# Optimization experiments

Hardware: AMD Instinct MI355X
Metric: run time of the kernel (lower is better)

The kernel has to match this reference:

```python
import jax, jax.numpy as jnp
import numpy as np

B, N, C, H, KS = 4, 1024, 768, 12, 7
DFF = 4 * C
HD = C // H
EPS = 1e-5


def layernorm(x, g, b):
    mu = jnp.mean(x, axis=-1, keepdims=True)
    var = jnp.mean(jnp.square(x - mu), axis=-1, keepdims=True)
    return (x - mu) * jax.lax.rsqrt(var + EPS) * g + b


def setup_inputs() -> dict:
    key = jax.random.key(0)
    ks = jax.random.split(key, 16)
    s = 0.02
    return {
        "x": jax.random.normal(ks[0], (B, N, C), jnp.float32),
        "w_qkv": jax.random.normal(ks[1], (3 * C, C), jnp.float32) * s,
        "b_qkv": jnp.zeros((3 * C,), jnp.float32),
        "w_proj": jax.random.normal(ks[2], (C, C), jnp.float32) * s,
        "b_proj": jnp.zeros((C,), jnp.float32),
        "w_fc1": jax.random.normal(ks[3], (DFF, C), jnp.float32) * s,
        "b_fc1": jnp.zeros((DFF,), jnp.float32),
        "w_fc2": jax.random.normal(ks[4], (C, DFF), jnp.float32) * s,
        "b_fc2": jnp.zeros((C,), jnp.float32),
        "t_before": jnp.eye(H, dtype=jnp.float32) + s * jax.random.normal(ks[5], (H, H), jnp.float32),
        "t_after": jnp.eye(H, dtype=jnp.float32) + s * jax.random.normal(ks[6], (H, H), jnp.float32),
        "g1": jnp.ones((C,), jnp.float32), "be1": jnp.zeros((C,), jnp.float32),
        "g2": jnp.ones((C,), jnp.float32), "be2": jnp.zeros((C,), jnp.float32),
        "dw_w": jax.random.normal(ks[7], (C, 1, KS), jnp.float32) * s,
        "dw_b": jnp.zeros((C,), jnp.float32),
        "gm": jnp.ones((C,), jnp.float32), "bm": jnp.zeros((C,), jnp.float32),
    }


def reference(x, w_qkv, b_qkv, w_proj, b_proj, w_fc1, b_fc1, w_fc2, b_fc2,
              t_before, t_after, g1, be1, g2, be2, dw_w, dw_b, gm, bm):
    residual = x
    h = layernorm(x, g1, be1)
    qkv = h @ w_qkv.T + b_qkv                       # [B,N,3C]
    qkv = qkv.reshape(B, N, 3, H, HD).transpose(2, 0, 3, 1, 4)  # [3,B,H,N,HD]
    q, k, v = qkv[0], qkv[1], qkv[2]
    scale = HD ** -0.5
    attn = jnp.einsum('bhnd,bhmd->bhnm', q, k) * scale          # [B,H,N,N]
    # head mixing before softmax: attn_perm @ T_before.T over head dim
    attn = jnp.einsum('bhnm,gh->bgnm', attn, t_before)
    attn = jax.nn.softmax(attn, axis=-1)
    # head mixing after softmax
    attn = jnp.einsum('bhnm,gh->bgnm', attn, t_after)
    out = jnp.einsum('bhnm,bhmd->bhnd', attn, v)                 # [B,H,N,HD]
    out = out.transpose(0, 2, 1, 3).reshape(B, N, C)
    out = out @ w_proj.T + b_proj
    x = residual + out
    residual = x
    h = layernorm(x, g2, be2)
    # MLP transform: depthwise conv1d over tokens + layernorm
    ht = h.transpose(0, 2, 1)                                    # [B,C,N]
    ht = jax.lax.conv_general_dilated(
        ht, dw_w, window_strides=(1,), padding=[(KS // 2, KS // 2)],
        feature_group_count=C, dimension_numbers=('NCH', 'OIH', 'NCH'))
    ht = ht + dw_b[None, :, None]
    h = layernorm(ht.transpose(0, 2, 1), gm, bm)
    # standard MLP (fc1 -> GELU -> fc2)
    h = jax.nn.gelu(h @ w_fc1.T + b_fc1, approximate=False)
    h = h @ w_fc2.T + b_fc2
    return residual + h
```

## Files before the change

### kernel.cpp

```cpp
#include <hip/hip_runtime.h>


typedef unsigned short u16;
typedef __bf16 bf16x8 __attribute__((ext_vector_type(8)));
typedef u16 u16x8 __attribute__((ext_vector_type(8)));
typedef float f32x4 __attribute__((ext_vector_type(4)));

using gvoid = __attribute__((address_space(1))) const void;
using lvoid = __attribute__((address_space(3))) void;
#define GLD16(GP, LP) __builtin_amdgcn_global_load_lds((gvoid*)(GP), (lvoid*)(LP), 16, 0, 0)

__device__ __forceinline__ u16 f2b(float f) {
  unsigned u = __float_as_uint(f);
  u = (u + 0x7FFFu + ((u >> 16) & 1u)) >> 16;
  return (u16)u;
}
__device__ __forceinline__ float b2f(u16 b) { return __uint_as_float(((unsigned)b) << 16); }
__device__ __forceinline__ float gelu_exact(float x) {
  return 0.5f * x * (1.f + erff(x * 0.70710678118654752f));
}
__device__ __forceinline__ unsigned pk2(float a, float b) {
  return (unsigned)f2b(a) | ((unsigned)f2b(b) << 16);
}

__global__ __launch_bounds__(256) void cast_all(const float* __restrict__ s0,
                                                const float* __restrict__ s1,
                                                const float* __restrict__ s2,
                                                const float* __restrict__ s3,
                                                u16* __restrict__ d0, u16* __restrict__ d1,
                                                u16* __restrict__ d2, u16* __restrict__ d3) {
  const int n0 = 1769472 / 4, n1 = 589824 / 4, n2 = 2359296 / 4;
  int j = blockIdx.x * 256 + threadIdx.x;
  const float* src;
  u16* dst;
  if (j < n0) { src = s0; dst = d0; }
  else if ((j -= n0) < n1) { src = s1; dst = d1; }
  else if ((j -= n1) < n2) { src = s2; dst = d2; }
  else { j -= n2; src = s3; dst = d3; }
  const float4 v = ((const float4*)src)[j];
  ushort4 o;
  o.x = f2b(v.x); o.y = f2b(v.y); o.z = f2b(v.z); o.w = f2b(v.w);
  ((ushort4*)dst)[j] = o;
}

template <typename OutT>
__global__ __launch_bounds__(256) void ln_row(const float* __restrict__ x,
                                              const float* __restrict__ g,
                                              const float* __restrict__ be,
                                              OutT* __restrict__ out) {
  const long row = blockIdx.x;
  const float* xr = x + row * 768;
  OutT* yr = out + row * 768;
  const int tid = threadIdx.x;
  const int w = tid >> 6, lane = tid & 63;
  float v[3], s = 0.f, s2 = 0.f;
#pragma unroll
  for (int i = 0; i < 3; ++i) {
    v[i] = xr[tid + i * 256];
    s += v[i];
    s2 += v[i] * v[i];
  }
#pragma unroll
  for (int off = 32; off; off >>= 1) {
    s += __shfl_xor(s, off);
    s2 += __shfl_xor(s2, off);
  }
  __shared__ float red[8];
  if (lane == 0) { red[w] = s; red[w + 4] = s2; }
  __syncthreads();
  s = red[0] + red[1] + red[2] + red[3];
  s2 = red[4] + red[5] + red[6] + red[7];
  const float mu = s * (1.f / 768.f);
  const float var = s2 * (1.f / 768.f) - mu * mu;
  const float rstd = rsqrtf(var + 1e-5f);
#pragma unroll
  for (int i = 0; i < 3; ++i) {
    const int c = tid + i * 256;
    float y = (v[i] - mu) * rstd * g[c] + be[c];
    if constexpr (sizeof(OutT) == 2) yr[c] = f2b(y);
    else yr[c] = y;
  }
}

template <int TM, int TN, int ACT, bool HAS_RES, typename OutT>
__global__ __launch_bounds__(256) void gemm_bt(
    const u16* __restrict__ A, const u16* __restrict__ B, OutT* __restrict__ C,
    const float* __restrict__ bias, const float* __restrict__ res,
    int K, int lda, int ldb, int ldc, int ldr) {
  constexpr int WM = TM / 2, WN = TN / 2, MR = WM / 16, NR = WN / 16;
  __shared__ __align__(16) u16 As[2][TM * 32];
  __shared__ __align__(16) u16 Bs[2][TN * 32];
  const int tid = threadIdx.x;
  const int w = tid >> 6, lane = tid & 63;
  const int wr = w >> 1, wc = w & 1;
  const int l16 = lane & 15, lh = lane >> 4;
  const long rowA = (long)blockIdx.y * TM;
  const long colB = (long)blockIdx.x * TN;
  const int srow = tid >> 2;
  const int scol = (((tid & 3) ^ (srow & 3))) * 8;

  f32x4 acc[NR][MR];
#pragma unroll
  for (int n = 0; n < NR; ++n)
#pragma unroll
    for (int m = 0; m < MR; ++m) acc[n][m] = f32x4{0.f, 0.f, 0.f, 0.f};

  auto stage = [&](int buf, int k0) {
#pragma unroll
    for (int r = 0; r < TM / 64; ++r)
      GLD16(A + (rowA + r * 64 + srow) * (long)lda + k0 + scol, (char*)As[buf] + r * 4096 + w * 1024);
#pragma unroll
    for (int r = 0; r < TN / 64; ++r)
      GLD16(B + (colB + r * 64 + srow) * (long)ldb + k0 + scol, (char*)Bs[buf] + r * 4096 + w * 1024);
  };

  stage(0, 0);
  __syncthreads();
  const int nk = K >> 5;
  const int rx = (lh ^ (l16 & 3)) * 8;
  for (int t = 0; t < nk; ++t) {
    const int buf = t & 1;
    if (t + 1 < nk) stage(buf ^ 1, (t + 1) << 5);
    bf16x8 a[MR], bb[NR];
#pragma unroll
    for (int m = 0; m < MR; ++m)
      a[m] = *(const bf16x8*)&As[buf][(wr * WM + m * 16 + l16) * 32 + rx];
#pragma unroll
    for (int n = 0; n < NR; ++n)
      bb[n] = *(const bf16x8*)&Bs[buf][(wc * WN + n * 16 + l16) * 32 + rx];
#pragma unroll
    for (int n = 0; n < NR; ++n)
#pragma unroll
      for (int m = 0; m < MR; ++m)
        acc[n][m] = __builtin_amdgcn_mfma_f32_16x16x32_bf16(bb[n], a[m], acc[n][m], 0, 0, 0);
    __syncthreads();
  }

  const long row0 = rowA + wr * WM;
  const long col0 = colB + wc * WN;
#pragma unroll
  for (int m = 0; m < MR; ++m) {
    const long row = row0 + m * 16 + l16;
#pragma unroll
    for (int n = 0; n < NR; ++n) {
      const long colb = col0 + n * 16 + lh * 4;
      f32x4 v = acc[n][m];
      if (bias) {
        const float4 bv = *(const float4*)&bias[colb];
        v[0] += bv.x; v[1] += bv.y; v[2] += bv.z; v[3] += bv.w;
      }
      if (ACT == 1) {
#pragma unroll
        for (int r = 0; r < 4; ++r) v[r] = gelu_exact(v[r]);
      }
      if (HAS_RES) {
        const float4 rv = *(const float4*)&res[row * (long)ldr + colb];
        v[0] += rv.x; v[1] += rv.y; v[2] += rv.z; v[3] += rv.w;
      }
      if constexpr (sizeof(OutT) == 2) {
        uint2 d;
        d.x = pk2(v[0], v[1]);
        d.y = pk2(v[2], v[3]);
        *(uint2*)&C[row * (long)ldc + colb] = d;
      } else {
        float4 d = {v[0], v[1], v[2], v[3]};
        *(float4*)&C[row * (long)ldc + colb] = d;
      }
    }
  }
}

__global__ __launch_bounds__(256) void scores_mix(const u16* __restrict__ qkv,
                                                  const float* __restrict__ Tb,
                                                  u16* __restrict__ attn) {
  __shared__ float Ts[144];
  const int tid = threadIdx.x;
  if (tid < 144) Ts[tid] = Tb[tid];
  __syncthreads();
  const int w = tid >> 6, lane = tid & 63;
  const int l16 = lane & 15, lh = lane >> 4;
  const int b = blockIdx.z;
  const int m0 = blockIdx.x * 64 + (w & 1) * 32;
  const int n0 = blockIdx.y * 32 + (w >> 1) * 16;
  const char* qb = (const char*)qkv;
  const long qrow = ((long)(b << 10) + n0 + l16) * 4608 + lh * 16;
  const long krow0 = ((long)(b << 10) + m0 + l16) * 4608 + 1536 + lh * 16;
  const long krow1 = krow0 + 16 * 4608;

  f32x4 acc[12][2];
#pragma unroll
  for (int h = 0; h < 12; ++h) {
    acc[h][0] = f32x4{0.f, 0.f, 0.f, 0.f};
    acc[h][1] = f32x4{0.f, 0.f, 0.f, 0.f};
  }
#pragma unroll
  for (int h = 0; h < 12; ++h)
#pragma unroll
    for (int kk = 0; kk < 2; ++kk) {
      const int off = h * 128 + kk * 64;
      const bf16x8 q  = *(const bf16x8*)(qb + qrow + off);
      const bf16x8 k0 = *(const bf16x8*)(qb + krow0 + off);
      const bf16x8 k1 = *(const bf16x8*)(qb + krow1 + off);
      acc[h][0] = __builtin_amdgcn_mfma_f32_16x16x32_bf16(k0, q, acc[h][0], 0, 0, 0);
      acc[h][1] = __builtin_amdgcn_mfma_f32_16x16x32_bf16(k1, q, acc[h][1], 0, 0, 0);
    }
  u16* abase = attn + (((long)(b * 12)) << 20) + (long)(n0 + l16) * 1024 + m0 + lh * 4;
#pragma unroll
  for (int g = 0; g < 12; ++g) {
    f32x4 o0 = f32x4{0.f, 0.f, 0.f, 0.f};
    f32x4 o1 = f32x4{0.f, 0.f, 0.f, 0.f};
#pragma unroll
    for (int h = 0; h < 12; ++h) {
      const float t = Ts[g * 12 + h];
      o0 += t * acc[h][0];
      o1 += t * acc[h][1];
    }
    uint2 d0, d1;
    d0.x = pk2(o0[0] * 0.125f, o0[1] * 0.125f);
    d0.y = pk2(o0[2] * 0.125f, o0[3] * 0.125f);
    d1.x = pk2(o1[0] * 0.125f, o1[1] * 0.125f);
    d1.y = pk2(o1[2] * 0.125f, o1[3] * 0.125f);
    u16* dst = abase + ((long)g << 20);
    *(uint2*)dst = d0;
    *(uint2*)(dst + 16) = d1;
  }
}

__global__ __launch_bounds__(256) void softmax_mix(u16* __restrict__ attn,
                                                   const float* __restrict__ Tg) {
  const int bi = blockIdx.x >> 10;
  const int n = blockIdx.x & 1023;
  __shared__ float Ta[144];
  __shared__ float red[8];
  const int tid = threadIdx.x;
  const int w = tid >> 6, lane = tid & 63;
  if (tid < 144) Ta[tid] = Tg[tid];
  const long base = (((long)bi * 12) << 20) + (long)n * 1024;
  float p[12][4];
#pragma unroll
  for (int h = 0; h < 12; ++h) {
    const uint2 d = ((const uint2*)(attn + base + ((long)h << 20)))[tid];
    float v[4] = {b2f((u16)(d.x & 0xffff)), b2f((u16)(d.x >> 16)),
                  b2f((u16)(d.y & 0xffff)), b2f((u16)(d.y >> 16))};
    float mx = fmaxf(fmaxf(v[0], v[1]), fmaxf(v[2], v[3]));
#pragma unroll
    for (int off = 32; off; off >>= 1) mx = fmaxf(mx, __shfl_xor(mx, off));
    __syncthreads();
    if (lane == 0) red[w] = mx;
    __syncthreads();
    mx = fmaxf(fmaxf(red[0], red[1]), fmaxf(red[2], red[3]));
    float s = 0.f;
#pragma unroll
    for (int i = 0; i < 4; ++i) {
      v[i] = __expf(v[i] - mx);
      s += v[i];
    }
#pragma unroll
    for (int off = 32; off; off >>= 1) s += __shfl_xor(s, off);
    if (lane == 0) red[w + 4] = s;
    __syncthreads();
    s = red[4] + red[5] + red[6] + red[7];
    const float inv = 1.f / s;
#pragma unroll
    for (int i = 0; i < 4; ++i) p[h][i] = v[i] * inv;
  }
#pragma unroll
  for (int g = 0; g < 12; ++g) {
    float o[4] = {0.f, 0.f, 0.f, 0.f};
#pragma unroll
    for (int h = 0; h < 12; ++h) {
      const float t = Ta[g * 12 + h];
#pragma unroll
      for (int i = 0; i < 4; ++i) o[i] += t * p[h][i];
    }
    uint2 d;
    d.x = pk2(o[0], o[1]);
    d.y = pk2(o[2], o[3]);
    ((uint2*)(attn + base + ((long)g << 20)))[tid] = d;
  }
}

__global__ __launch_bounds__(256) void av_gemm(const u16* __restrict__ attn,
                                               const u16* __restrict__ qkv,
                                               u16* __restrict__ out) {
  __shared__ __align__(16) u16 As[2][64 * 32];
  __shared__ __align__(16) u16 Vt[2][64 * 40];
  const int tid = threadIdx.x;
  const int w = tid >> 6, lane = tid & 63;
  const int z = blockIdx.y, b = z / 12, h = z % 12;
  const u16* A = attn + ((long)z << 20);
  const u16* V = qkv + (long)b * 1024 * 2304 + 1536 + h * 64;
  const int rowA = blockIdx.x * 64;
  const int srow = tid >> 2;
  const int scol = (((tid & 3) ^ (srow & 3))) * 8;
  const int l16 = lane & 15, lh = lane >> 4;

  f32x4 acc[4];
#pragma unroll
  for (int n = 0; n < 4; ++n) acc[n] = f32x4{0.f, 0.f, 0.f, 0.f};

  auto stageA = [&](int buf, int k0) {
    GLD16(A + (long)(rowA + srow) * 1024 + k0 + scol, (char*)As[buf] + w * 1024);
  };
  auto stageV = [&](int buf, int k0) {
    u16x8 tmp;
#pragma unroll
    for (int j = 0; j < 8; ++j) tmp[j] = V[(long)(k0 + w * 8 + j) * 2304 + lane];
    *(u16x8*)&Vt[buf][lane * 40 + w * 8] = tmp;
  };

  stageA(0, 0);
  stageV(0, 0);
  __syncthreads();
  for (int t = 0; t < 32; ++t) {
    const int buf = t & 1;
    if (t < 31) { stageA(buf ^ 1, (t + 1) * 32); stageV(buf ^ 1, (t + 1) * 32); }
    const bf16x8 a = *(const bf16x8*)&As[buf][(w * 16 + l16) * 32 + (lh ^ (l16 & 3)) * 8];
    bf16x8 bv[4];
#pragma unroll
    for (int n = 0; n < 4; ++n)
      bv[n] = *(const bf16x8*)&Vt[buf][(n * 16 + l16) * 40 + lh * 8];
#pragma unroll
    for (int n = 0; n < 4; ++n)
      acc[n] = __builtin_amdgcn_mfma_f32_16x16x32_bf16(bv[n], a, acc[n], 0, 0, 0);
    __syncthreads();
  }
  const int tok = rowA + w * 16 + l16;
  u16* obase = out + ((long)(b << 10) + tok) * 768 + h * 64 + lh * 4;
#pragma unroll
  for (int df = 0; df < 4; ++df) {
    uint2 d;
    d.x = pk2(acc[df][0], acc[df][1]);
    d.y = pk2(acc[df][2], acc[df][3]);
    *(uint2*)(obase + df * 16) = d;
  }
}

__global__ __launch_bounds__(256) void dwconv4(const float* __restrict__ h2,
                                               const float* __restrict__ wgt,
                                               const float* __restrict__ bias,
                                               float* __restrict__ ct) {
  const int idx = blockIdx.x * 256 + threadIdx.x;
  const int c4 = idx % 192;
  const int n = (idx / 192) % 1024;
  const int b = idx / (192 * 1024);
  const int c = c4 * 4;
  float4 acc = ((const float4*)bias)[c4];
#pragma unroll
  for (int t = 0; t < 7; ++t) {
    const int nn = n + t - 3;
    if (nn >= 0 && nn < 1024) {
      const float4 v = *(const float4*)&h2[((long)(b << 10) + nn) * 768 + c];
      acc.x += v.x * wgt[(c + 0) * 7 + t];
      acc.y += v.y * wgt[(c + 1) * 7 + t];
      acc.z += v.z * wgt[(c + 2) * 7 + t];
      acc.w += v.w * wgt[(c + 3) * 7 + t];
    }
  }
  ((float4*)ct)[idx] = acc;
}

extern "C" void kernel_launch(void* const* d_in, const int* in_sizes, int n_in,
                              void* d_out, int out_size, void* d_ws, size_t ws_size,
                              hipStream_t stream) {
  const float* x      = (const float*)d_in[0];
  const float* w_qkv  = (const float*)d_in[1];
  const float* b_qkv  = (const float*)d_in[2];
  const float* w_proj = (const float*)d_in[3];
  const float* b_proj = (const float*)d_in[4];
  const float* w_fc1  = (const float*)d_in[5];
  const float* b_fc1  = (const float*)d_in[6];
  const float* w_fc2  = (const float*)d_in[7];
  const float* b_fc2  = (const float*)d_in[8];
  const float* t_bef  = (const float*)d_in[9];
  const float* t_aft  = (const float*)d_in[10];
  const float* g1     = (const float*)d_in[11];
  const float* be1    = (const float*)d_in[12];
  const float* g2     = (const float*)d_in[13];
  const float* be2    = (const float*)d_in[14];
  const float* dw_w   = (const float*)d_in[15];
  const float* dw_b   = (const float*)d_in[16];
  const float* gm     = (const float*)d_in[17];
  const float* bm     = (const float*)d_in[18];
  float* out = (float*)d_out;

  char* wsp = (char*)d_ws;
  size_t off = 0;
  auto alloc = [&](size_t bytes) {
    char* r = wsp + off;
    off += (bytes + 255) & ~(size_t)255;
    return r;
  };
  u16* wqkv_b  = (u16*)alloc((size_t)2304 * 768 * 2);
  u16* wproj_b = (u16*)alloc((size_t)768 * 768 * 2);
  u16* wfc1_b  = (u16*)alloc((size_t)3072 * 768 * 2);
  u16* wfc2_b  = (u16*)alloc((size_t)768 * 3072 * 2);
  u16* h1      = (u16*)alloc((size_t)4096 * 768 * 2);
  u16* attn_out = h1;
  u16* qkvb    = (u16*)alloc((size_t)4096 * 2304 * 2);
  char* attn_region = alloc((size_t)48 * 1024 * 1024 * 2);
  u16* attn = (u16*)attn_region;
  size_t ro = 0;
  auto ralloc = [&](size_t bytes) {
    char* r = attn_region + ro;
    ro += (bytes + 255) & ~(size_t)255;
    return r;
  };
  float* x2   = (float*)ralloc((size_t)4096 * 768 * 4);
  float* h2   = (float*)ralloc((size_t)4096 * 768 * 4);
  float* ct   = (float*)ralloc((size_t)4096 * 768 * 4);
  u16*   hm   = (u16*)ralloc((size_t)4096 * 768 * 2);
  u16*   fc1o = (u16*)ralloc((size_t)4096 * 3072 * 2);
  (void)ws_size; (void)n_in; (void)in_sizes; (void)out_size;

  cast_all<<<6912, 256, 0, stream>>>(w_qkv, w_proj, w_fc1, w_fc2,
                                     wqkv_b, wproj_b, wfc1_b, wfc2_b);
  ln_row<u16><<<4096, 256, 0, stream>>>(x, g1, be1, h1);
  gemm_bt<128, 64, 0, false, u16><<<dim3(36, 32), 256, 0, stream>>>(
      h1, wqkv_b, qkvb, b_qkv, nullptr, 768, 768, 768, 2304, 0);
  scores_mix<<<dim3(16, 32, 4), 256, 0, stream>>>(qkvb, t_bef, attn);
  softmax_mix<<<4096, 256, 0, stream>>>(attn, t_aft);
  av_gemm<<<dim3(16, 48), 256, 0, stream>>>(attn, qkvb, attn_out);
  gemm_bt<64, 64, 0, true, float><<<dim3(12, 64), 256, 0, stream>>>(
      attn_out, wproj_b, x2, b_proj, x, 768, 768, 768, 768, 768);
  ln_row<float><<<4096, 256, 0, stream>>>(x2, g2, be2, h2);
  dwconv4<<<3072, 256, 0, stream>>>(h2, dw_w, dw_b, ct);
  ln_row<u16><<<4096, 256, 0, stream>>>(ct, gm, bm, hm);
  gemm_bt<128, 64, 1, false, u16><<<dim3(48, 32), 256, 0, stream>>>(
      hm, wfc1_b, fc1o, b_fc1, nullptr, 768, 768, 768, 3072, 0);
  gemm_bt<64, 64, 0, true, float><<<dim3(12, 64), 256, 0, stream>>>(
      fc1o, wfc2_b, out, b_fc2, x2, 3072, 3072, 3072, 768, 768);
}
```

Before: 485.8 us.

## Stage Q/K tiles in LDS with double-buffered async loads in scores_mix

The scores_mix kernel now stages per-head Q and K tiles into swizzled shared memory using global_load_lds with a two-buffer pipeline, instead of each wave reading fragments straight from global memory. The head mixing is applied incrementally per head into 12 output accumulators, and the 0.125 scale is folded into the mixing matrix. This cuts redundant global reads across waves and overlaps loading with MFMA work, at the cost of a barrier per head and extra LDS usage.

```diff
diff --git a/kernel.cpp b/kernel.cpp
--- a/kernel.cpp
+++ b/kernel.cpp
@@ -173,53 +173,73 @@
 __global__ __launch_bounds__(256) void scores_mix(const u16* __restrict__ qkv,
                                                   const float* __restrict__ Tb,
                                                   u16* __restrict__ attn) {
+  __shared__ __align__(16) u16 Qs[2][32 * 64];
+  __shared__ __align__(16) u16 Ks[2][64 * 64];
   __shared__ float Ts[144];
   const int tid = threadIdx.x;
-  if (tid < 144) Ts[tid] = Tb[tid];
+  const int w = tid >> 6, lane = tid & 63;
+  if (tid < 144) Ts[tid] = Tb[tid] * 0.125f;
+  const int b = blockIdx.z;
+  const int m0 = blockIdx.x * 64;
+  const int n0 = blockIdx.y * 32;
+  const int mb = (w & 1) * 32, nb = (w >> 1) * 16;
+  const int l16 = lane & 15, lh = lane >> 4;
+
+  const int sr = tid >> 3, sc = tid & 7;
+  const long qsrc = ((long)(b << 10) + n0 + sr) * 2304 + (sc ^ (sr & 7)) * 8;
+  const long ksrc0 = ((long)(b << 10) + m0 + sr) * 2304 + 768 + (sc ^ (sr & 7)) * 8;
+  const long ksrc1 = ((long)(b << 10) + m0 + 32 + sr) * 2304 + 768 + (sc ^ ((32 + sr) & 7)) * 8;
+
+  auto stage = [&](int buf, int h) {
+    GLD16(qkv + qsrc + h * 64, (char*)Qs[buf] + w * 1024);
+    GLD16(qkv + ksrc0 + h * 64, (char*)Ks[buf] + w * 1024);
+    GLD16(qkv + ksrc1 + h * 64, (char*)Ks[buf] + 4096 + w * 1024);
+  };
+
+  f32x4 o[12][2];
+#pragma unroll
+  for (int g = 0; g < 12; ++g) {
+    o[g][0] = f32x4{0.f, 0.f, 0.f, 0.f};
+    o[g][1] = f32x4{0.f, 0.f, 0.f, 0.f};
+  }
+
+  stage(0, 0);
   __syncthreads();
-  const int w = tid >> 6, lane = tid & 63;
-  const int l16 = lane & 15, lh = lane >> 4;
-  const int b = blockIdx.z;
-  const int m0 = blockIdx.x * 64 + (w & 1) * 32;
-  const int n0 = blockIdx.y * 32 + (w >> 1) * 16;
-  const char* qb = (const char*)qkv;
-  const long qrow = ((long)(b << 10) + n0 + l16) * 4608 + lh * 16;
-  const long krow0 = ((long)(b << 10) + m0 + l16) * 4608 + 1536 + lh * 16;
-  const long krow1 = krow0 + 16 * 4608;
-
-  f32x4 acc[12][2];
-#pragma unroll
+  const int qrow = nb + l16;
+  const int krow0 = mb + l16, krow1 = mb + 16 + l16;
   for (int h = 0; h < 12; ++h) {
-    acc[h][0] = f32x4{0.f, 0.f, 0.f, 0.f};
-    acc[h][1] = f32x4{0.f, 0.f, 0.f, 0.f};
-  }
-#pragma unroll
-  for (int h = 0; h < 12; ++h)
+    const int buf = h & 1;
+    if (h < 11) stage(buf ^ 1, h + 1);
+    f32x4 s0 = f32x4{0.f, 0.f, 0.f, 0.f};
+    f32x4 s1 = f32x4{0.f, 0.f, 0.f, 0.f};
 #pragma unroll
     for (int kk = 0; kk < 2; ++kk) {
-      const int off = h * 128 + kk * 64;
-      const bf16x8 q  = *(const bf16x8*)(qb + qrow + off);
-      const bf16x8 k0 = *(const bf16x8*)(qb + krow0 + off);
-      const bf16x8 k1 = *(const bf16x8*)(qb + krow1 + off);
-      acc[h][0] = __builtin_amdgcn_mfma_f32_16x16x32_bf16(k0, q, acc[h][0], 0, 0, 0);
-      acc[h][1] = __builtin_amdgcn_mfma_f32_16x16x32_bf16(k1, q, acc[h][1], 0, 0, 0);
-    }
-  u16* abase = attn + (((long)(b * 12)) << 20) + (long)(n0 + l16) * 1024 + m0 + lh * 4;
+      const int g4 = (kk << 2) | lh;
+      const bf16x8 qf = *(const bf16x8*)&Qs[buf][qrow * 64 + (g4 ^ (qrow & 7)) * 8];
+      const bf16x8 k0 = *(const bf16x8*)&Ks[buf][krow0 * 64 + (g4 ^ (krow0 & 7)) * 8];
+      const bf16x8 k1 = *(const bf16x8*)&Ks[buf][krow1 * 64 + (g4 ^ (krow1 & 7)) * 8];
+      s0 = __builtin_amdgcn_mfma_f32_16x16x32_bf16(k0, qf, s0, 0, 0, 0);
+      s1 = __builtin_amdgcn_mfma_f32_16x16x32_bf16(k1, qf, s1, 0, 0, 0);
+    }
+#pragma unroll
+    for (int g = 0; g < 12; ++g) {
+      const float t = Ts[g * 12 + h];
+      o[g][0] += t * s0;
+      o[g][1] += t * s1;
+    }
+    __syncthreads();
+  }
+
+  const int gn = n0 + nb + l16;
+  const int gm = m0 + mb + lh * 4;
+  u16* abase = attn + (((long)(b * 12)) << 20) + (long)gn * 1024 + gm;
 #pragma unroll
   for (int g = 0; g < 12; ++g) {
-    f32x4 o0 = f32x4{0.f, 0.f, 0.f, 0.f};
-    f32x4 o1 = f32x4{0.f, 0.f, 0.f, 0.f};
-#pragma unroll
-    for (int h = 0; h < 12; ++h) {
-      const float t = Ts[g * 12 + h];
-      o0 += t * acc[h][0];
-      o1 += t * acc[h][1];
-    }
     uint2 d0, d1;
-    d0.x = pk2(o0[0] * 0.125f, o0[1] * 0.125f);
-    d0.y = pk2(o0[2] * 0.125f, o0[3] * 0.125f);
-    d1.x = pk2(o1[0] * 0.125f, o1[1] * 0.125f);
-    d1.y = pk2(o1[2] * 0.125f, o1[3] * 0.125f);
+    d0.x = pk2(o[g][0][0], o[g][0][1]);
+    d0.y = pk2(o[g][0][2], o[g][0][3]);
+    d1.x = pk2(o[g][1][0], o[g][1][1]);
+    d1.y = pk2(o[g][1][2], o[g][1][3]);
     u16* dst = abase + ((long)g << 20);
     *(uint2*)dst = d0;
     *(uint2*)(dst + 16) = d1;
```

After: 498.3 us. 2.6% more time.

## Split per-head score GEMM with LDS tiling; move pre-softmax head mix into softmax

Applied to the files above, without the earlier changes.

The scores kernel now computes raw per-head QK^T tiles (128x64 per block) using swizzled LDS staging via global_load_lds, instead of holding all 12 heads in registers and mixing them there. The pre-softmax head mixing by T_before moves into the softmax kernel, which now applies both mixes to the values it already reads. The proj and fc2 GEMMs also switch to 128-row tiles. The goal is better K/Q reuse and less register pressure in the scores kernel. In exchange the raw scores are rounded to bf16 before mixing, which may change accuracy slightly, and the softmax kernel does more arithmetic.

```diff
diff --git a/kernel.cpp b/kernel.cpp
--- a/kernel.cpp
+++ b/kernel.cpp
@@ -170,78 +170,108 @@
   }
 }
 
-__global__ __launch_bounds__(256) void scores_mix(const u16* __restrict__ qkv,
-                                                  const float* __restrict__ Tb,
+__global__ __launch_bounds__(256) void scores_raw(const u16* __restrict__ qkv,
                                                   u16* __restrict__ attn) {
-  __shared__ float Ts[144];
+  __shared__ __align__(16) u16 Ks[128 * 64];
+  __shared__ __align__(16) u16 Qs[64 * 64];
   const int tid = threadIdx.x;
-  if (tid < 144) Ts[tid] = Tb[tid];
+  const int w = tid >> 6, lane = tid & 63;
+  const int z = blockIdx.z, b = z / 12, h = z % 12;
+  const int m0 = blockIdx.x * 128, n0 = blockIdx.y * 64;
+  const int l16 = lane & 15, lh = lane >> 4;
+  const int sr = tid >> 3, sc = tid & 7;
+  const u16* Kb = qkv + ((long)(b << 10)) * 2304 + 768 + h * 64;
+  const u16* Qb = qkv + ((long)(b << 10)) * 2304 + h * 64;
+#pragma unroll
+  for (int i = 0; i < 4; ++i) {
+    const int r = i * 32 + sr;
+    GLD16(Kb + (long)(m0 + r) * 2304 + (sc ^ (r & 7)) * 8, (char*)Ks + i * 4096 + w * 1024);
+  }
+#pragma unroll
+  for (int i = 0; i < 2; ++i) {
+    const int r = i * 32 + sr;
+    GLD16(Qb + (long)(n0 + r) * 2304 + (sc ^ (r & 7)) * 8, (char*)Qs + i * 4096 + w * 1024);
+  }
   __syncthreads();
-  const int w = tid >> 6, lane = tid & 63;
-  const int l16 = lane & 15, lh = lane >> 4;
-  const int b = blockIdx.z;
-  const int m0 = blockIdx.x * 64 + (w & 1) * 32;
-  const int n0 = blockIdx.y * 32 + (w >> 1) * 16;
-  const char* qb = (const char*)qkv;
-  const long qrow = ((long)(b << 10) + n0 + l16) * 4608 + lh * 16;
-  const long krow0 = ((long)(b << 10) + m0 + l16) * 4608 + 1536 + lh * 16;
-  const long krow1 = krow0 + 16 * 4608;
-
-  f32x4 acc[12][2];
-#pragma unroll
-  for (int h = 0; h < 12; ++h) {
-    acc[h][0] = f32x4{0.f, 0.f, 0.f, 0.f};
-    acc[h][1] = f32x4{0.f, 0.f, 0.f, 0.f};
-  }
-#pragma unroll
-  for (int h = 0; h < 12; ++h)
-#pragma unroll
-    for (int kk = 0; kk < 2; ++kk) {
-      const int off = h * 128 + kk * 64;
-      const bf16x8 q  = *(const bf16x8*)(qb + qrow + off);
-      const bf16x8 k0 = *(const bf16x8*)(qb + krow0 + off);
-      const bf16x8 k1 = *(const bf16x8*)(qb + krow1 + off);
-      acc[h][0] = __builtin_amdgcn_mfma_f32_16x16x32_bf16(k0, q, acc[h][0], 0, 0, 0);
-      acc[h][1] = __builtin_amdgcn_mfma_f32_16x16x32_bf16(k1, q, acc[h][1], 0, 0, 0);
-    }
-  u16* abase = attn + (((long)(b * 12)) << 20) + (long)(n0 + l16) * 1024 + m0 + lh * 4;
-#pragma unroll
-  for (int g = 0; g < 12; ++g) {
-    f32x4 o0 = f32x4{0.f, 0.f, 0.f, 0.f};
-    f32x4 o1 = f32x4{0.f, 0.f, 0.f, 0.f};
-#pragma unroll
-    for (int h = 0; h < 12; ++h) {
-      const float t = Ts[g * 12 + h];
-      o0 += t * acc[h][0];
-      o1 += t * acc[h][1];
-    }
-    uint2 d0, d1;
-    d0.x = pk2(o0[0] * 0.125f, o0[1] * 0.125f);
-    d0.y = pk2(o0[2] * 0.125f, o0[3] * 0.125f);
-    d1.x = pk2(o1[0] * 0.125f, o1[1] * 0.125f);
-    d1.y = pk2(o1[2] * 0.125f, o1[3] * 0.125f);
-    u16* dst = abase + ((long)g << 20);
-    *(uint2*)dst = d0;
-    *(uint2*)(dst + 16) = d1;
+  const int mb = (w & 1) * 64, nb = (w >> 1) * 32;
+  f32x4 acc[2][4];
+#pragma unroll
+  for (int n = 0; n < 2; ++n)
+#pragma unroll
+    for (int m = 0; m < 4; ++m) acc[n][m] = f32x4{0.f, 0.f, 0.f, 0.f};
+#pragma unroll
+  for (int kk = 0; kk < 2; ++kk) {
+    bf16x8 kf[4], qf[2];
+    const int g4 = (kk << 2) | lh;
+#pragma unroll
+    for (int mf = 0; mf < 4; ++mf) {
+      const int row = mb + mf * 16 + l16;
+      kf[mf] = *(const bf16x8*)&Ks[row * 64 + (g4 ^ (row & 7)) * 8];
+    }
+#pragma unroll
+    for (int nf = 0; nf < 2; ++nf) {
+      const int row = nb + nf * 16 + l16;
+      qf[nf] = *(const bf16x8*)&Qs[row * 64 + (g4 ^ (row & 7)) * 8];
+    }
+#pragma unroll
+    for (int nf = 0; nf < 2; ++nf)
+#pragma unroll
+      for (int mf = 0; mf < 4; ++mf)
+        acc[nf][mf] = __builtin_amdgcn_mfma_f32_16x16x32_bf16(kf[mf], qf[nf], acc[nf][mf], 0, 0, 0);
+  }
+  const long gbase = ((long)z << 20);
+#pragma unroll
+  for (int nf = 0; nf < 2; ++nf) {
+    const int n = n0 + nb + nf * 16 + l16;
+    u16* dst = attn + gbase + (long)n * 1024 + m0 + mb + lh * 4;
+#pragma unroll
+    for (int mf = 0; mf < 4; ++mf) {
+      uint2 d;
+      d.x = pk2(acc[nf][mf][0] * 0.125f, acc[nf][mf][1] * 0.125f);
+      d.y = pk2(acc[nf][mf][2] * 0.125f, acc[nf][mf][3] * 0.125f);
+      *(uint2*)(dst + mf * 16) = d;
+    }
   }
 }
 
 __global__ __launch_bounds__(256) void softmax_mix(u16* __restrict__ attn,
-                                                   const float* __restrict__ Tg) {
+                                                   const float* __restrict__ TbM,
+                                                   const float* __restrict__ TgM) {
   const int bi = blockIdx.x >> 10;
   const int n = blockIdx.x & 1023;
-  __shared__ float Ta[144];
+  __shared__ float Ts[144], Ta[144];
   __shared__ float red[8];
   const int tid = threadIdx.x;
   const int w = tid >> 6, lane = tid & 63;
-  if (tid < 144) Ta[tid] = Tg[tid];
+  if (tid < 144) { Ts[tid] = TbM[tid]; Ta[tid] = TgM[tid]; }
+  __syncthreads();
   const long base = (((long)bi * 12) << 20) + (long)n * 1024;
-  float p[12][4];
+  float raw[12][4];
 #pragma unroll
   for (int h = 0; h < 12; ++h) {
     const uint2 d = ((const uint2*)(attn + base + ((long)h << 20)))[tid];
-    float v[4] = {b2f((u16)(d.x & 0xffff)), b2f((u16)(d.x >> 16)),
-                  b2f((u16)(d.y & 0xffff)), b2f((u16)(d.y >> 16))};
+    raw[h][0] = b2f((u16)(d.x & 0xffff));
+    raw[h][1] = b2f((u16)(d.x >> 16));
+    raw[h][2] = b2f((u16)(d.y & 0xffff));
+    raw[h][3] = b2f((u16)(d.y >> 16));
+  }
+  float p[12][4];
+#pragma unroll
+  for (int g = 0; g < 12; ++g) {
+    float o0 = 0.f, o1 = 0.f, o2 = 0.f, o3 = 0.f;
+#pragma unroll
+    for (int h = 0; h < 12; ++h) {
+      const float t = Ts[g * 12 + h];
+      o0 += t * raw[h][0];
+      o1 += t * raw[h][1];
+      o2 += t * raw[h][2];
+      o3 += t * raw[h][3];
+    }
+    p[g][0] = o0; p[g][1] = o1; p[g][2] = o2; p[g][3] = o3;
+  }
+#pragma unroll
+  for (int g = 0; g < 12; ++g) {
+    float v[4] = {p[g][0], p[g][1], p[g][2], p[g][3]};
     float mx = fmaxf(fmaxf(v[0], v[1]), fmaxf(v[2], v[3]));
 #pragma unroll
     for (int off = 32; off; off >>= 1) mx = fmaxf(mx, __shfl_xor(mx, off));
@@ -262,7 +292,7 @@
     s = red[4] + red[5] + red[6] + red[7];
     const float inv = 1.f / s;
 #pragma unroll
-    for (int i = 0; i < 4; ++i) p[h][i] = v[i] * inv;
+    for (int i = 0; i < 4; ++i) p[g][i] = v[i] * inv;
   }
 #pragma unroll
   for (int g = 0; g < 12; ++g) {
@@ -418,16 +448,16 @@
   ln_row<u16><<<4096, 256, 0, stream>>>(x, g1, be1, h1);
   gemm_bt<128, 64, 0, false, u16><<<dim3(36, 32), 256, 0, stream>>>(
       h1, wqkv_b, qkvb, b_qkv, nullptr, 768, 768, 768, 2304, 0);
-  scores_mix<<<dim3(16, 32, 4), 256, 0, stream>>>(qkvb, t_bef, attn);
-  softmax_mix<<<4096, 256, 0, stream>>>(attn, t_aft);
+  scores_raw<<<dim3(8, 16, 48), 256, 0, stream>>>(qkvb, attn);
+  softmax_mix<<<4096, 256, 0, stream>>>(attn, t_bef, t_aft);
   av_gemm<<<dim3(16, 48), 256, 0, stream>>>(attn, qkvb, attn_out);
-  gemm_bt<64, 64, 0, true, float><<<dim3(12, 64), 256, 0, stream>>>(
+  gemm_bt<128, 64, 0, true, float><<<dim3(12, 32), 256, 0, stream>>>(
       attn_out, wproj_b, x2, b_proj, x, 768, 768, 768, 768, 768);
   ln_row<float><<<4096, 256, 0, stream>>>(x2, g2, be2, h2);
   dwconv4<<<3072, 256, 0, stream>>>(h2, dw_w, dw_b, ct);
   ln_row<u16><<<4096, 256, 0, stream>>>(ct, gm, bm, hm);
   gemm_bt<128, 64, 1, false, u16><<<dim3(48, 32), 256, 0, stream>>>(
       hm, wfc1_b, fc1o, b_fc1, nullptr, 768, 768, 768, 3072, 0);
-  gemm_bt<64, 64, 0, true, float><<<dim3(12, 64), 256, 0, stream>>>(
+  gemm_bt<128, 64, 0, true, float><<<dim3(12, 32), 256, 0, stream>>>(
       fc1o, wfc2_b, out, b_fc2, x2, 3072, 3072, 3072, 768, 768);
 }
```

After: 481.3 us. About the same (-0.9%).
